# Kernel optimization log

Hardware: AMD Instinct MI355X
Metric: run time of the kernel (lower is better)

The kernel has to match this reference:

```python
import jax, jax.numpy as jnp
import numpy as np

B, N, CQ, H, CH = 1, 256, 128, 4, 32  # batch, n_res, c_q(=c_k=c_v), heads, per-head dim


def setup_inputs() -> dict:
    key = jax.random.key(0)
    ks = jax.random.split(key, 12)
    s = 0.02
    q_x = jax.random.normal(ks[0], (B, N, N, CQ), jnp.float32)
    kv_x = jax.random.normal(ks[1], (B, N, N, CQ), jnp.float32)
    # mask bias: 0 where kept, -1e9 where masked (additive mask)
    keep = jax.random.uniform(ks[2], (B, N, 1, 1, N)) < 0.9
    mask_bias = jnp.where(keep, 0.0, -1e9).astype(jnp.float32)
    triangle_bias = jax.random.normal(ks[3], (B, 1, H, N, N), jnp.float32)
    # projection weights, stored per-head as [H, CH, C_in]
    wq = jax.random.normal(ks[4], (H, CH, CQ), jnp.float32) * s
    wk = jax.random.normal(ks[5], (H, CH, CQ), jnp.float32) * s
    wv = jax.random.normal(ks[6], (H, CH, CQ), jnp.float32) * s
    wg = jax.random.normal(ks[7], (H, CH, CQ), jnp.float32) * s
    bg = jax.random.normal(ks[8], (H, CH), jnp.float32) * s + 1.0  # gating bias init 1
    wo = jax.random.normal(ks[9], (CQ, H * CH), jnp.float32) * s
    bo = jnp.zeros((CQ,), jnp.float32)
    return {"q_x": q_x, "kv_x": kv_x, "mask_bias": mask_bias,
            "triangle_bias": triangle_bias, "wq": wq, "wk": wk, "wv": wv,
            "wg": wg, "bg": bg, "wo": wo, "bo": bo}


def reference(q_x, kv_x, mask_bias, triangle_bias, wq, wk, wv, wg, bg, wo, bo):
    scale = 1.0 / np.sqrt(CH).astype(np.float32)
    # project + split heads: [B,N,Q,C] x [H,D,C] -> [B,N,H,Q,D]
    q = jnp.einsum('bnqc,hdc->bnhqd', q_x, wq) * scale
    k = jnp.einsum('bnkc,hdc->bnhkd', kv_x, wk)
    v = jnp.einsum('bnkc,hdc->bnhkd', kv_x, wv)
    # scores + additive biases (mask_bias broadcasts over h,q; triangle over n)
    a = jnp.einsum('bnhqd,bnhkd->bnhqk', q, k) + mask_bias + triangle_bias
    a = jax.nn.softmax(a, axis=-1)
    o = jnp.einsum('bnhqk,bnhkd->bnhqd', a, v)
    o = jnp.swapaxes(o, -2, -3)  # [B,N,Q,H,D]
    # gating
    g = jax.nn.sigmoid(jnp.einsum('bnqc,hdc->bnqhd', q_x, wg) + bg)
    o = o * g
    o = o.reshape(o.shape[:-2] + (H * CH,))  # [B,N,Q,H*D]
    return jnp.einsum('bnqe,ce->bnqc', o, wo) + bo
```

## Files before the change

### kernel.cpp

```cpp
#include <hip/hip_runtime.h>

#define NRES 256
#define CIN  128
#define NH   4
#define DH   32

typedef __attribute__((ext_vector_type(4))) float f32x4;
typedef __attribute__((ext_vector_type(8))) short bf16x8;

__device__ __forceinline__ short f2bf(float f) {
    unsigned u = __builtin_bit_cast(unsigned, f);
    u = (u + 0x7fffu + ((u >> 16) & 1u)) >> 16;
    return (short)u;
}

__device__ __forceinline__ bf16x8 ldcvt8(const float* __restrict__ p, float sc) {
    float4 a = *(const float4*)p;
    float4 b = *(const float4*)(p + 4);
    bf16x8 r;
    r[0] = f2bf(a.x * sc); r[1] = f2bf(a.y * sc); r[2] = f2bf(a.z * sc); r[3] = f2bf(a.w * sc);
    r[4] = f2bf(b.x * sc); r[5] = f2bf(b.y * sc); r[6] = f2bf(b.z * sc); r[7] = f2bf(b.w * sc);
    return r;
}

#define MFMA(a, b, c) __builtin_amdgcn_mfma_f32_16x16x32_bf16((a), (b), (c), 0, 0, 0)

__global__ __launch_bounds__(256, 2) void attn_mfma(
    const float* __restrict__ q_x, const float* __restrict__ kv_x,
    const float* __restrict__ mask_bias, const float* __restrict__ tri_bias,
    const float* __restrict__ wq, const float* __restrict__ wk,
    const float* __restrict__ wv, float* __restrict__ o_out)
{
    const int h = blockIdx.x, n = blockIdx.y;
    const int t = threadIdx.x;
    const int lane = t & 63, w = t >> 6;
    const int mrow = lane & 15;
    const int grp  = lane >> 4;
    const int koff = grp * 8;
    const int rbase = grp * 4;
    const int q0 = w * 64;

    __shared__ unsigned short Qs[NRES * DH];
    __shared__ unsigned short Ks[NRES * DH];
    __shared__ unsigned short Vt[DH * NRES];
    __shared__ unsigned short Pt[4 * 16 * 32];
    __shared__ float msk[NRES];

    if (t < 64) *(float4*)&msk[t * 4] = *(const float4*)(mask_bias + n * NRES + t * 4);

    const float* __restrict__ qxn  = q_x  + (size_t)n * NRES * CIN;
    const float* __restrict__ kxn  = kv_x + (size_t)n * NRES * CIN;
    const float* __restrict__ wqh  = wq + h * DH * CIN;
    const float* __restrict__ wkh  = wk + h * DH * CIN;
    const float* __restrict__ wvh  = wv + h * DH * CIN;
    const float* __restrict__ trih = tri_bias + (size_t)h * NRES * NRES;

    {
        const float qsc = 0.17677669529663687f;
        f32x4 aq_[4][2], ak_[4][2], av_[4][2];
        const f32x4 zf = {0.f, 0.f, 0.f, 0.f};
        #pragma unroll
        for (int qt = 0; qt < 4; ++qt)
            for (int dt = 0; dt < 2; ++dt) { aq_[qt][dt] = zf; ak_[qt][dt] = zf; av_[qt][dt] = zf; }

        #pragma unroll
        for (int ct = 0; ct < 4; ++ct) {
            const int c0 = ct * 32 + koff;
            bf16x8 bq0 = ldcvt8(wqh + mrow * CIN + c0, qsc);
            bf16x8 bq1 = ldcvt8(wqh + (16 + mrow) * CIN + c0, qsc);
            bf16x8 bk0 = ldcvt8(wkh + mrow * CIN + c0, 1.f);
            bf16x8 bk1 = ldcvt8(wkh + (16 + mrow) * CIN + c0, 1.f);
            bf16x8 bv0 = ldcvt8(wvh + mrow * CIN + c0, 1.f);
            bf16x8 bv1 = ldcvt8(wvh + (16 + mrow) * CIN + c0, 1.f);
            #pragma unroll
            for (int qt = 0; qt < 4; ++qt) {
                bf16x8 aX = ldcvt8(qxn + (q0 + qt * 16 + mrow) * CIN + c0, 1.f);
                aq_[qt][0] = MFMA(aX, bq0, aq_[qt][0]);
                aq_[qt][1] = MFMA(aX, bq1, aq_[qt][1]);
                bf16x8 aK = ldcvt8(kxn + (q0 + qt * 16 + mrow) * CIN + c0, 1.f);
                ak_[qt][0] = MFMA(aK, bk0, ak_[qt][0]);
                ak_[qt][1] = MFMA(aK, bk1, ak_[qt][1]);
                av_[qt][0] = MFMA(aK, bv0, av_[qt][0]);
                av_[qt][1] = MFMA(aK, bv1, av_[qt][1]);
            }
        }
        #pragma unroll
        for (int qt = 0; qt < 4; ++qt)
            #pragma unroll
            for (int dt = 0; dt < 2; ++dt)
                #pragma unroll
                for (int r = 0; r < 4; ++r) {
                    const int row = q0 + qt * 16 + rbase + r;
                    const int d = dt * 16 + mrow;
                    Qs[row * DH + d]   = (unsigned short)f2bf(aq_[qt][dt][r]);
                    Ks[row * DH + d]   = (unsigned short)f2bf(ak_[qt][dt][r]);
                    Vt[d * NRES + row] = (unsigned short)f2bf(av_[qt][dt][r]);
                }
    }
    __syncthreads();

    bf16x8 aq[4];
    #pragma unroll
    for (int qt = 0; qt < 4; ++qt)
        aq[qt] = *(const bf16x8*)&Qs[(q0 + qt * 16 + mrow) * DH + koff];

    f32x4 oa[4][2];
    f32x4 ls[4];
    const f32x4 zf = {0.f, 0.f, 0.f, 0.f};
    #pragma unroll
    for (int qt = 0; qt < 4; ++qt) { oa[qt][0] = zf; oa[qt][1] = zf; ls[qt] = zf; }

    unsigned short* __restrict__ pw = &Pt[w * 512];

    for (int kt = 0; kt < 8; ++kt) {
        const int kb = kt * 32;
        bf16x8 bk0 = *(const bf16x8*)&Ks[(kb + mrow) * DH + koff];
        bf16x8 bk1 = *(const bf16x8*)&Ks[(kb + 16 + mrow) * DH + koff];
        bf16x8 bv0 = *(const bf16x8*)&Vt[mrow * NRES + kb + koff];
        bf16x8 bv1 = *(const bf16x8*)&Vt[(16 + mrow) * NRES + kb + koff];
        const float mb0 = msk[kb + mrow];
        const float mb1 = msk[kb + 16 + mrow];

        #pragma unroll
        for (int qt = 0; qt < 4; ++qt) {
            f32x4 s0 = MFMA(aq[qt], bk0, zf);
            f32x4 s1 = MFMA(aq[qt], bk1, zf);
            const float* __restrict__ trow =
                trih + (q0 + qt * 16 + rbase) * NRES + kb + mrow;
            #pragma unroll
            for (int r = 0; r < 4; ++r) {
                s0[r] = __expf(s0[r] + mb0 + trow[r * NRES]      - 8.f);
                s1[r] = __expf(s1[r] + mb1 + trow[r * NRES + 16] - 8.f);
            }
            ls[qt] += s0 + s1;
            #pragma unroll
            for (int r = 0; r < 4; ++r) {
                pw[(rbase + r) * 32 + mrow]      = (unsigned short)f2bf(s0[r]);
                pw[(rbase + r) * 32 + 16 + mrow] = (unsigned short)f2bf(s1[r]);
            }
            asm volatile("s_waitcnt lgkmcnt(0)" ::: "memory");
            bf16x8 pa = *(const bf16x8*)&pw[mrow * 32 + koff];
            oa[qt][0] = MFMA(pa, bv0, oa[qt][0]);
            oa[qt][1] = MFMA(pa, bv1, oa[qt][1]);
        }
    }

    float* __restrict__ orow = o_out + (size_t)n * NRES * CIN + h * DH;
    #pragma unroll
    for (int qt = 0; qt < 4; ++qt) {
        f32x4 lv = ls[qt];
        #pragma unroll
        for (int xm = 1; xm < 16; xm <<= 1) {
            lv[0] += __shfl_xor(lv[0], xm, 64);
            lv[1] += __shfl_xor(lv[1], xm, 64);
            lv[2] += __shfl_xor(lv[2], xm, 64);
            lv[3] += __shfl_xor(lv[3], xm, 64);
        }
        #pragma unroll
        for (int r = 0; r < 4; ++r) {
            const float iv = 1.f / lv[r];
            const int q = q0 + qt * 16 + rbase + r;
            orow[q * CIN + mrow]      = oa[qt][0][r] * iv;
            orow[q * CIN + 16 + mrow] = oa[qt][1][r] * iv;
        }
    }
}

__global__ __launch_bounds__(256, 2) void gate_out(
    const float* __restrict__ q_x, const float* __restrict__ wg,
    const float* __restrict__ bg, const float* __restrict__ wo,
    const float* __restrict__ bo, float* __restrict__ io)
{
    const int t = threadIdx.x;
    const int tn = t & 31;
    const int tm = t >> 5;
    const int r0 = blockIdx.x * 64;

    __shared__ float As[64 * 128];
    __shared__ float Bs[16 * 128];

    {
        const int row = t >> 2, c0 = (t & 3) * 32;
        const float* __restrict__ src = q_x + (size_t)(r0 + row) * CIN + c0;
        #pragma unroll
        for (int p = 0; p < 8; ++p)
            *(float4*)&As[row * 128 + c0 + p * 4] = *(const float4*)(src + p * 4);
    }
    __syncthreads();

    float acc[8][4];
    #pragma unroll
    for (int i = 0; i < 8; ++i)
        #pragma unroll
        for (int j = 0; j < 4; ++j) acc[i][j] = 0.f;

    for (int kc = 0; kc < 8; ++kc) {
        {
            const int e = t >> 1, ch = (t & 1) * 8;
            const float* __restrict__ sw = wg + e * CIN + kc * 16 + ch;
            float4 v0 = *(const float4*)sw, v1 = *(const float4*)(sw + 4);
            Bs[(ch + 0) * 128 + e] = v0.x; Bs[(ch + 1) * 128 + e] = v0.y;
            Bs[(ch + 2) * 128 + e] = v0.z; Bs[(ch + 3) * 128 + e] = v0.w;
            Bs[(ch + 4) * 128 + e] = v1.x; Bs[(ch + 5) * 128 + e] = v1.y;
            Bs[(ch + 6) * 128 + e] = v1.z; Bs[(ch + 7) * 128 + e] = v1.w;
        }
        __syncthreads();
        #pragma unroll
        for (int kk = 0; kk < 16; ++kk) {
            float4 b4 = *(const float4*)&Bs[kk * 128 + tn * 4];
            #pragma unroll
            for (int i = 0; i < 8; ++i) {
                const float a = As[(tm * 8 + i) * 128 + kc * 16 + kk];
                acc[i][0] += a * b4.x; acc[i][1] += a * b4.y;
                acc[i][2] += a * b4.z; acc[i][3] += a * b4.w;
            }
        }
        __syncthreads();
    }

    float4 bg4 = *(const float4*)(bg + tn * 4);
    float gated[8][4];
    #pragma unroll
    for (int i = 0; i < 8; ++i) {
        float4 ov = *(const float4*)(io + (size_t)(r0 + tm * 8 + i) * CIN + tn * 4);
        const float o_[4] = {ov.x, ov.y, ov.z, ov.w};
        const float b_[4] = {bg4.x, bg4.y, bg4.z, bg4.w};
        #pragma unroll
        for (int j = 0; j < 4; ++j) {
            const float g = 1.f / (1.f + __expf(-(acc[i][j] + b_[j])));
            gated[i][j] = o_[j] * g;
        }
    }
    __syncthreads();
    #pragma unroll
    for (int i = 0; i < 8; ++i)
        *(float4*)&As[(tm * 8 + i) * 128 + tn * 4] =
            make_float4(gated[i][0], gated[i][1], gated[i][2], gated[i][3]);
    __syncthreads();

    float acc2[8][4];
    #pragma unroll
    for (int i = 0; i < 8; ++i)
        #pragma unroll
        for (int j = 0; j < 4; ++j) acc2[i][j] = 0.f;

    for (int kc = 0; kc < 8; ++kc) {
        {
            const int c = t >> 1, eh = (t & 1) * 8;
            const float* __restrict__ sw = wo + c * 128 + kc * 16 + eh;
            float4 v0 = *(const float4*)sw, v1 = *(const float4*)(sw + 4);
            Bs[(eh + 0) * 128 + c] = v0.x; Bs[(eh + 1) * 128 + c] = v0.y;
            Bs[(eh + 2) * 128 + c] = v0.z; Bs[(eh + 3) * 128 + c] = v0.w;
            Bs[(eh + 4) * 128 + c] = v1.x; Bs[(eh + 5) * 128 + c] = v1.y;
            Bs[(eh + 6) * 128 + c] = v1.z; Bs[(eh + 7) * 128 + c] = v1.w;
        }
        __syncthreads();
        #pragma unroll
        for (int kk = 0; kk < 16; ++kk) {
            float4 b4 = *(const float4*)&Bs[kk * 128 + tn * 4];
            #pragma unroll
            for (int i = 0; i < 8; ++i) {
                const float a = As[(tm * 8 + i) * 128 + kc * 16 + kk];
                acc2[i][0] += a * b4.x; acc2[i][1] += a * b4.y;
                acc2[i][2] += a * b4.z; acc2[i][3] += a * b4.w;
            }
        }
        __syncthreads();
    }

    float4 bo4 = *(const float4*)(bo + tn * 4);
    #pragma unroll
    for (int i = 0; i < 8; ++i) {
        float4 v = make_float4(acc2[i][0] + bo4.x, acc2[i][1] + bo4.y,
                               acc2[i][2] + bo4.z, acc2[i][3] + bo4.w);
        *(float4*)(io + (size_t)(r0 + tm * 8 + i) * CIN + tn * 4) = v;
    }
}

extern "C" void kernel_launch(void* const* d_in, const int* in_sizes, int n_in,
                              void* d_out, int out_size, void* d_ws, size_t ws_size,
                              hipStream_t stream) {
    const float* q_x  = (const float*)d_in[0];
    const float* kv_x = (const float*)d_in[1];
    const float* mask = (const float*)d_in[2];
    const float* tri  = (const float*)d_in[3];
    const float* wq   = (const float*)d_in[4];
    const float* wk   = (const float*)d_in[5];
    const float* wv   = (const float*)d_in[6];
    const float* wg   = (const float*)d_in[7];
    const float* bg   = (const float*)d_in[8];
    const float* wo   = (const float*)d_in[9];
    const float* bo   = (const float*)d_in[10];
    float* out = (float*)d_out;

    attn_mfma<<<dim3(NH, NRES), 256, 0, stream>>>(q_x, kv_x, mask, tri, wq, wk, wv, out);
    gate_out<<<(NRES * NRES) / 64, 256, 0, stream>>>(q_x, wg, bg, wo, bo, out);
}
```

Before: 263.0 us.

## Port gate/output projection to bf16 MFMA and restructure attention LDS usage

The gating and output projection kernel moves from a scalar fp32 shared-memory GEMM to bf16 MFMA, with gated activations staged per wave in padded LDS and launched with 128 rows per block. The attention kernel drops the shared Q buffer and passes Q through per-wave scratch instead. It also pads the V and P LDS strides, batches the triangle-bias loads ahead of the score MFMAs, packs bf16 conversions with perm, and raises the occupancy hint. The gate path gives up fp32 accuracy for bf16 matmuls, and the weights are reloaded from global memory for every tile.

```diff
diff --git a/kernel.cpp b/kernel.cpp
--- a/kernel.cpp
+++ b/kernel.cpp
@@ -5,27 +5,43 @@
 #define NH   4
 #define DH   32
 
+#define KST 32
+#define VST 264
+#define PST 40
+#define GST 136
+
 typedef __attribute__((ext_vector_type(4))) float f32x4;
 typedef __attribute__((ext_vector_type(8))) short bf16x8;
 
-__device__ __forceinline__ short f2bf(float f) {
+__device__ __forceinline__ unsigned pkbf(float a, float b) {
+    unsigned ua = __builtin_bit_cast(unsigned, a);
+    unsigned ub = __builtin_bit_cast(unsigned, b);
+    ua += 0x7fffu + ((ua >> 16) & 1u);
+    ub += 0x7fffu + ((ub >> 16) & 1u);
+    return __builtin_amdgcn_perm(ub, ua, 0x07060302);
+}
+__device__ __forceinline__ unsigned short f2bfu(float f) {
     unsigned u = __builtin_bit_cast(unsigned, f);
-    u = (u + 0x7fffu + ((u >> 16) & 1u)) >> 16;
-    return (short)u;
-}
-
-__device__ __forceinline__ bf16x8 ldcvt8(const float* __restrict__ p, float sc) {
-    float4 a = *(const float4*)p;
-    float4 b = *(const float4*)(p + 4);
-    bf16x8 r;
-    r[0] = f2bf(a.x * sc); r[1] = f2bf(a.y * sc); r[2] = f2bf(a.z * sc); r[3] = f2bf(a.w * sc);
-    r[4] = f2bf(b.x * sc); r[5] = f2bf(b.y * sc); r[6] = f2bf(b.z * sc); r[7] = f2bf(b.w * sc);
-    return r;
-}
-
+    return (unsigned short)((u + 0x7fffu + ((u >> 16) & 1u)) >> 16);
+}
+union bfr { unsigned u[4]; bf16x8 v; };
+__device__ __forceinline__ bf16x8 ldcvt8(const float* __restrict__ p) {
+    f32x4 a = *(const f32x4*)p; f32x4 b = *(const f32x4*)(p + 4);
+    bfr r;
+    r.u[0] = pkbf(a[0], a[1]); r.u[1] = pkbf(a[2], a[3]);
+    r.u[2] = pkbf(b[0], b[1]); r.u[3] = pkbf(b[2], b[3]);
+    return r.v;
+}
+__device__ __forceinline__ bf16x8 ldcvt8s(const float* __restrict__ p, float sc) {
+    f32x4 a = *(const f32x4*)p; f32x4 b = *(const f32x4*)(p + 4);
+    bfr r;
+    r.u[0] = pkbf(a[0] * sc, a[1] * sc); r.u[1] = pkbf(a[2] * sc, a[3] * sc);
+    r.u[2] = pkbf(b[0] * sc, b[1] * sc); r.u[3] = pkbf(b[2] * sc, b[3] * sc);
+    return r.v;
+}
 #define MFMA(a, b, c) __builtin_amdgcn_mfma_f32_16x16x32_bf16((a), (b), (c), 0, 0, 0)
 
-__global__ __launch_bounds__(256, 2) void attn_mfma(
+__global__ __launch_bounds__(256, 3) void attn_mfma(
     const float* __restrict__ q_x, const float* __restrict__ kv_x,
     const float* __restrict__ mask_bias, const float* __restrict__ tri_bias,
     const float* __restrict__ wq, const float* __restrict__ wk,
@@ -40,115 +56,143 @@
     const int rbase = grp * 4;
     const int q0 = w * 64;
 
-    __shared__ unsigned short Qs[NRES * DH];
-    __shared__ unsigned short Ks[NRES * DH];
-    __shared__ unsigned short Vt[DH * NRES];
-    __shared__ unsigned short Pt[4 * 16 * 32];
+    __shared__ unsigned short Ks[NRES * KST];
+    __shared__ unsigned short Vt[DH * VST];
+    __shared__ unsigned short Pt[4 * 32 * PST];
     __shared__ float msk[NRES];
 
     if (t < 64) *(float4*)&msk[t * 4] = *(const float4*)(mask_bias + n * NRES + t * 4);
 
-    const float* __restrict__ qxn  = q_x  + (size_t)n * NRES * CIN;
-    const float* __restrict__ kxn  = kv_x + (size_t)n * NRES * CIN;
-    const float* __restrict__ wqh  = wq + h * DH * CIN;
-    const float* __restrict__ wkh  = wk + h * DH * CIN;
-    const float* __restrict__ wvh  = wv + h * DH * CIN;
-    const float* __restrict__ trih = tri_bias + (size_t)h * NRES * NRES;
-
-    {
-        const float qsc = 0.17677669529663687f;
-        f32x4 aq_[4][2], ak_[4][2], av_[4][2];
-        const f32x4 zf = {0.f, 0.f, 0.f, 0.f};
-        #pragma unroll
-        for (int qt = 0; qt < 4; ++qt)
-            for (int dt = 0; dt < 2; ++dt) { aq_[qt][dt] = zf; ak_[qt][dt] = zf; av_[qt][dt] = zf; }
-
-        #pragma unroll
-        for (int ct = 0; ct < 4; ++ct) {
-            const int c0 = ct * 32 + koff;
-            bf16x8 bq0 = ldcvt8(wqh + mrow * CIN + c0, qsc);
-            bf16x8 bq1 = ldcvt8(wqh + (16 + mrow) * CIN + c0, qsc);
-            bf16x8 bk0 = ldcvt8(wkh + mrow * CIN + c0, 1.f);
-            bf16x8 bk1 = ldcvt8(wkh + (16 + mrow) * CIN + c0, 1.f);
-            bf16x8 bv0 = ldcvt8(wvh + mrow * CIN + c0, 1.f);
-            bf16x8 bv1 = ldcvt8(wvh + (16 + mrow) * CIN + c0, 1.f);
-            #pragma unroll
-            for (int qt = 0; qt < 4; ++qt) {
-                bf16x8 aX = ldcvt8(qxn + (q0 + qt * 16 + mrow) * CIN + c0, 1.f);
-                aq_[qt][0] = MFMA(aX, bq0, aq_[qt][0]);
-                aq_[qt][1] = MFMA(aX, bq1, aq_[qt][1]);
-                bf16x8 aK = ldcvt8(kxn + (q0 + qt * 16 + mrow) * CIN + c0, 1.f);
-                ak_[qt][0] = MFMA(aK, bk0, ak_[qt][0]);
-                ak_[qt][1] = MFMA(aK, bk1, ak_[qt][1]);
-                av_[qt][0] = MFMA(aK, bv0, av_[qt][0]);
-                av_[qt][1] = MFMA(aK, bv1, av_[qt][1]);
-            }
-        }
-        #pragma unroll
-        for (int qt = 0; qt < 4; ++qt)
+    const float* __restrict__ qxn = q_x  + (size_t)n * NRES * CIN;
+    const float* __restrict__ kxn = kv_x + (size_t)n * NRES * CIN;
+    const float* __restrict__ wqh = wq + h * DH * CIN;
+    const float* __restrict__ wkh = wk + h * DH * CIN;
+    const float* __restrict__ wvh = wv + h * DH * CIN;
+
+    f32x4 aq_[4][2], ak_[4][2], av_[4][2];
+    const f32x4 zf = {0.f, 0.f, 0.f, 0.f};
+    #pragma unroll
+    for (int qt = 0; qt < 4; ++qt)
+        #pragma unroll
+        for (int dt = 0; dt < 2; ++dt) { aq_[qt][dt] = zf; ak_[qt][dt] = zf; av_[qt][dt] = zf; }
+
+    const float qsc = 0.17677669529663687f;
+    #pragma unroll
+    for (int ct = 0; ct < 4; ++ct) {
+        const int c0 = ct * 32 + koff;
+        bf16x8 bq0 = ldcvt8s(wqh + mrow * CIN + c0, qsc);
+        bf16x8 bq1 = ldcvt8s(wqh + (16 + mrow) * CIN + c0, qsc);
+        bf16x8 bk0 = ldcvt8(wkh + mrow * CIN + c0);
+        bf16x8 bk1 = ldcvt8(wkh + (16 + mrow) * CIN + c0);
+        bf16x8 bv0 = ldcvt8(wvh + mrow * CIN + c0);
+        bf16x8 bv1 = ldcvt8(wvh + (16 + mrow) * CIN + c0);
+        #pragma unroll
+        for (int qt = 0; qt < 4; ++qt) {
+            bf16x8 aX = ldcvt8(qxn + (q0 + qt * 16 + mrow) * CIN + c0);
+            aq_[qt][0] = MFMA(aX, bq0, aq_[qt][0]);
+            aq_[qt][1] = MFMA(aX, bq1, aq_[qt][1]);
+            bf16x8 aK = ldcvt8(kxn + (q0 + qt * 16 + mrow) * CIN + c0);
+            ak_[qt][0] = MFMA(aK, bk0, ak_[qt][0]);
+            ak_[qt][1] = MFMA(aK, bk1, ak_[qt][1]);
+            av_[qt][0] = MFMA(aK, bv0, av_[qt][0]);
+            av_[qt][1] = MFMA(aK, bv1, av_[qt][1]);
+        }
+    }
+
+    #pragma unroll
+    for (int qt = 0; qt < 4; ++qt)
+        #pragma unroll
+        for (int dt = 0; dt < 2; ++dt)
+            #pragma unroll
+            for (int r = 0; r < 4; ++r) {
+                const int row = q0 + qt * 16 + rbase + r;
+                const int d = dt * 16 + mrow;
+                Ks[row * KST + d] = f2bfu(ak_[qt][dt][r]);
+                Vt[d * VST + row] = f2bfu(av_[qt][dt][r]);
+            }
+
+    unsigned short* __restrict__ pw = &Pt[w * 32 * PST];
+    bf16x8 aq[4];
+    #pragma unroll
+    for (int h2 = 0; h2 < 2; ++h2) {
+        #pragma unroll
+        for (int j = 0; j < 2; ++j) {
+            const int qt = h2 * 2 + j;
             #pragma unroll
             for (int dt = 0; dt < 2; ++dt)
                 #pragma unroll
-                for (int r = 0; r < 4; ++r) {
-                    const int row = q0 + qt * 16 + rbase + r;
-                    const int d = dt * 16 + mrow;
-                    Qs[row * DH + d]   = (unsigned short)f2bf(aq_[qt][dt][r]);
-                    Ks[row * DH + d]   = (unsigned short)f2bf(ak_[qt][dt][r]);
-                    Vt[d * NRES + row] = (unsigned short)f2bf(av_[qt][dt][r]);
-                }
+                for (int r = 0; r < 4; ++r)
+                    pw[(j * 16 + rbase + r) * PST + dt * 16 + mrow] = f2bfu(aq_[qt][dt][r]);
+        }
+        asm volatile("s_waitcnt lgkmcnt(0)" ::: "memory");
+        #pragma unroll
+        for (int j = 0; j < 2; ++j)
+            aq[h2 * 2 + j] = *(const bf16x8*)&pw[(j * 16 + mrow) * PST + koff];
+        asm volatile("s_waitcnt lgkmcnt(0)" ::: "memory");
     }
     __syncthreads();
 
-    bf16x8 aq[4];
-    #pragma unroll
-    for (int qt = 0; qt < 4; ++qt)
-        aq[qt] = *(const bf16x8*)&Qs[(q0 + qt * 16 + mrow) * DH + koff];
-
-    f32x4 oa[4][2];
-    f32x4 ls[4];
-    const f32x4 zf = {0.f, 0.f, 0.f, 0.f};
-    #pragma unroll
-    for (int qt = 0; qt < 4; ++qt) { oa[qt][0] = zf; oa[qt][1] = zf; ls[qt] = zf; }
-
-    unsigned short* __restrict__ pw = &Pt[w * 512];
+    f32x4 oa[4][2], ls4[4];
+    #pragma unroll
+    for (int qt = 0; qt < 4; ++qt) { oa[qt][0] = zf; oa[qt][1] = zf; ls4[qt] = zf; }
+
+    const float* __restrict__ trih = tri_bias + (size_t)h * NRES * NRES;
 
     for (int kt = 0; kt < 8; ++kt) {
         const int kb = kt * 32;
-        bf16x8 bk0 = *(const bf16x8*)&Ks[(kb + mrow) * DH + koff];
-        bf16x8 bk1 = *(const bf16x8*)&Ks[(kb + 16 + mrow) * DH + koff];
-        bf16x8 bv0 = *(const bf16x8*)&Vt[mrow * NRES + kb + koff];
-        bf16x8 bv1 = *(const bf16x8*)&Vt[(16 + mrow) * NRES + kb + koff];
-        const float mb0 = msk[kb + mrow];
-        const float mb1 = msk[kb + 16 + mrow];
-
-        #pragma unroll
-        for (int qt = 0; qt < 4; ++qt) {
-            f32x4 s0 = MFMA(aq[qt], bk0, zf);
-            f32x4 s1 = MFMA(aq[qt], bk1, zf);
-            const float* __restrict__ trow =
-                trih + (q0 + qt * 16 + rbase) * NRES + kb + mrow;
-            #pragma unroll
-            for (int r = 0; r < 4; ++r) {
-                s0[r] = __expf(s0[r] + mb0 + trow[r * NRES]      - 8.f);
-                s1[r] = __expf(s1[r] + mb1 + trow[r * NRES + 16] - 8.f);
-            }
-            ls[qt] += s0 + s1;
-            #pragma unroll
-            for (int r = 0; r < 4; ++r) {
-                pw[(rbase + r) * 32 + mrow]      = (unsigned short)f2bf(s0[r]);
-                pw[(rbase + r) * 32 + 16 + mrow] = (unsigned short)f2bf(s1[r]);
+        bf16x8 bk0 = *(const bf16x8*)&Ks[(kb + mrow) * KST + koff];
+        bf16x8 bk1 = *(const bf16x8*)&Ks[(kb + 16 + mrow) * KST + koff];
+        bf16x8 bv0 = *(const bf16x8*)&Vt[mrow * VST + kb + koff];
+        bf16x8 bv1 = *(const bf16x8*)&Vt[(16 + mrow) * VST + kb + koff];
+        const float mb0 = msk[kb + mrow] - 8.f;
+        const float mb1 = msk[kb + 16 + mrow] - 8.f;
+
+        #pragma unroll
+        for (int h2 = 0; h2 < 2; ++h2) {
+            float tr0[2][4], tr1[2][4];
+            #pragma unroll
+            for (int j = 0; j < 2; ++j) {
+                const int qt = h2 * 2 + j;
+                const float* __restrict__ trow =
+                    trih + (q0 + qt * 16 + rbase) * NRES + kb + mrow;
+                #pragma unroll
+                for (int r = 0; r < 4; ++r) {
+                    tr0[j][r] = trow[r * NRES];
+                    tr1[j][r] = trow[r * NRES + 16];
+                }
+            }
+            #pragma unroll
+            for (int j = 0; j < 2; ++j) {
+                const int qt = h2 * 2 + j;
+                f32x4 s0 = MFMA(aq[qt], bk0, zf);
+                f32x4 s1 = MFMA(aq[qt], bk1, zf);
+                #pragma unroll
+                for (int r = 0; r < 4; ++r) {
+                    s0[r] = __expf(s0[r] + tr0[j][r] + mb0);
+                    s1[r] = __expf(s1[r] + tr1[j][r] + mb1);
+                }
+                ls4[qt] += s0 + s1;
+                #pragma unroll
+                for (int r = 0; r < 4; ++r) {
+                    pw[(j * 16 + rbase + r) * PST + mrow]      = f2bfu(s0[r]);
+                    pw[(j * 16 + rbase + r) * PST + 16 + mrow] = f2bfu(s1[r]);
+                }
             }
             asm volatile("s_waitcnt lgkmcnt(0)" ::: "memory");
-            bf16x8 pa = *(const bf16x8*)&pw[mrow * 32 + koff];
-            oa[qt][0] = MFMA(pa, bv0, oa[qt][0]);
-            oa[qt][1] = MFMA(pa, bv1, oa[qt][1]);
+            #pragma unroll
+            for (int j = 0; j < 2; ++j) {
+                const int qt = h2 * 2 + j;
+                bf16x8 pa = *(const bf16x8*)&pw[(j * 16 + mrow) * PST + koff];
+                oa[qt][0] = MFMA(pa, bv0, oa[qt][0]);
+                oa[qt][1] = MFMA(pa, bv1, oa[qt][1]);
+            }
         }
     }
 
     float* __restrict__ orow = o_out + (size_t)n * NRES * CIN + h * DH;
     #pragma unroll
     for (int qt = 0; qt < 4; ++qt) {
-        f32x4 lv = ls[qt];
+        f32x4 lv = ls4[qt];
         #pragma unroll
         for (int xm = 1; xm < 16; xm <<= 1) {
             lv[0] += __shfl_xor(lv[0], xm, 64);
@@ -158,122 +202,91 @@
         }
         #pragma unroll
         for (int r = 0; r < 4; ++r) {
-            const float iv = 1.f / lv[r];
+            const float inv = 1.f / lv[r];
             const int q = q0 + qt * 16 + rbase + r;
-            orow[q * CIN + mrow]      = oa[qt][0][r] * iv;
-            orow[q * CIN + 16 + mrow] = oa[qt][1][r] * iv;
-        }
-    }
-}
-
-__global__ __launch_bounds__(256, 2) void gate_out(
+            orow[q * CIN + mrow]      = oa[qt][0][r] * inv;
+            orow[q * CIN + 16 + mrow] = oa[qt][1][r] * inv;
+        }
+    }
+}
+
+__global__ __launch_bounds__(256, 4) void gate_out(
     const float* __restrict__ q_x, const float* __restrict__ wg,
     const float* __restrict__ bg, const float* __restrict__ wo,
     const float* __restrict__ bo, float* __restrict__ io)
 {
     const int t = threadIdx.x;
-    const int tn = t & 31;
-    const int tm = t >> 5;
-    const int r0 = blockIdx.x * 64;
-
-    __shared__ float As[64 * 128];
-    __shared__ float Bs[16 * 128];
-
-    {
-        const int row = t >> 2, c0 = (t & 3) * 32;
-        const float* __restrict__ src = q_x + (size_t)(r0 + row) * CIN + c0;
-        #pragma unroll
-        for (int p = 0; p < 8; ++p)
-            *(float4*)&As[row * 128 + c0 + p * 4] = *(const float4*)(src + p * 4);
-    }
-    __syncthreads();
-
-    float acc[8][4];
-    #pragma unroll
-    for (int i = 0; i < 8; ++i)
-        #pragma unroll
-        for (int j = 0; j < 4; ++j) acc[i][j] = 0.f;
-
-    for (int kc = 0; kc < 8; ++kc) {
-        {
-            const int e = t >> 1, ch = (t & 1) * 8;
-            const float* __restrict__ sw = wg + e * CIN + kc * 16 + ch;
-            float4 v0 = *(const float4*)sw, v1 = *(const float4*)(sw + 4);
-            Bs[(ch + 0) * 128 + e] = v0.x; Bs[(ch + 1) * 128 + e] = v0.y;
-            Bs[(ch + 2) * 128 + e] = v0.z; Bs[(ch + 3) * 128 + e] = v0.w;
-            Bs[(ch + 4) * 128 + e] = v1.x; Bs[(ch + 5) * 128 + e] = v1.y;
-            Bs[(ch + 6) * 128 + e] = v1.z; Bs[(ch + 7) * 128 + e] = v1.w;
-        }
-        __syncthreads();
-        #pragma unroll
-        for (int kk = 0; kk < 16; ++kk) {
-            float4 b4 = *(const float4*)&Bs[kk * 128 + tn * 4];
-            #pragma unroll
-            for (int i = 0; i < 8; ++i) {
-                const float a = As[(tm * 8 + i) * 128 + kc * 16 + kk];
-                acc[i][0] += a * b4.x; acc[i][1] += a * b4.y;
-                acc[i][2] += a * b4.z; acc[i][3] += a * b4.w;
-            }
-        }
-        __syncthreads();
-    }
-
-    float4 bg4 = *(const float4*)(bg + tn * 4);
-    float gated[8][4];
-    #pragma unroll
-    for (int i = 0; i < 8; ++i) {
-        float4 ov = *(const float4*)(io + (size_t)(r0 + tm * 8 + i) * CIN + tn * 4);
-        const float o_[4] = {ov.x, ov.y, ov.z, ov.w};
-        const float b_[4] = {bg4.x, bg4.y, bg4.z, bg4.w};
-        #pragma unroll
-        for (int j = 0; j < 4; ++j) {
-            const float g = 1.f / (1.f + __expf(-(acc[i][j] + b_[j])));
-            gated[i][j] = o_[j] * g;
-        }
-    }
-    __syncthreads();
-    #pragma unroll
-    for (int i = 0; i < 8; ++i)
-        *(float4*)&As[(tm * 8 + i) * 128 + tn * 4] =
-            make_float4(gated[i][0], gated[i][1], gated[i][2], gated[i][3]);
-    __syncthreads();
-
-    float acc2[8][4];
-    #pragma unroll
-    for (int i = 0; i < 8; ++i)
-        #pragma unroll
-        for (int j = 0; j < 4; ++j) acc2[i][j] = 0.f;
-
-    for (int kc = 0; kc < 8; ++kc) {
-        {
-            const int c = t >> 1, eh = (t & 1) * 8;
-            const float* __restrict__ sw = wo + c * 128 + kc * 16 + eh;
-            float4 v0 = *(const float4*)sw, v1 = *(const float4*)(sw + 4);
-            Bs[(eh + 0) * 128 + c] = v0.x; Bs[(eh + 1) * 128 + c] = v0.y;
-            Bs[(eh + 2) * 128 + c] = v0.z; Bs[(eh + 3) * 128 + c] = v0.w;
-            Bs[(eh + 4) * 128 + c] = v1.x; Bs[(eh + 5) * 128 + c] = v1.y;
-            Bs[(eh + 6) * 128 + c] = v1.z; Bs[(eh + 7) * 128 + c] = v1.w;
-        }
-        __syncthreads();
-        #pragma unroll
-        for (int kk = 0; kk < 16; ++kk) {
-            float4 b4 = *(const float4*)&Bs[kk * 128 + tn * 4];
-            #pragma unroll
-            for (int i = 0; i < 8; ++i) {
-                const float a = As[(tm * 8 + i) * 128 + kc * 16 + kk];
-                acc2[i][0] += a * b4.x; acc2[i][1] += a * b4.y;
-                acc2[i][2] += a * b4.z; acc2[i][3] += a * b4.w;
-            }
-        }
-        __syncthreads();
-    }
-
-    float4 bo4 = *(const float4*)(bo + tn * 4);
-    #pragma unroll
-    for (int i = 0; i < 8; ++i) {
-        float4 v = make_float4(acc2[i][0] + bo4.x, acc2[i][1] + bo4.y,
-                               acc2[i][2] + bo4.z, acc2[i][3] + bo4.w);
-        *(float4*)(io + (size_t)(r0 + tm * 8 + i) * CIN + tn * 4) = v;
+    const int lane = t & 63, w = t >> 6;
+    const int mrow = lane & 15, grp = lane >> 4;
+    const int koff = grp * 8, rbase = grp * 4;
+    const int r0 = blockIdx.x * 128 + w * 32;
+
+    __shared__ unsigned short Gt[4 * 32 * GST];
+    unsigned short* __restrict__ gw = &Gt[w * 32 * GST];
+
+    const f32x4 zf = {0.f, 0.f, 0.f, 0.f};
+    f32x4 acc[2][8];
+    #pragma unroll
+    for (int at = 0; at < 2; ++at)
+        #pragma unroll
+        for (int nt = 0; nt < 8; ++nt) acc[at][nt] = zf;
+
+    #pragma unroll
+    for (int ks = 0; ks < 4; ++ks) {
+        const int c0 = ks * 32 + koff;
+        bf16x8 ax0 = ldcvt8(q_x + (size_t)(r0 + mrow) * CIN + c0);
+        bf16x8 ax1 = ldcvt8(q_x + (size_t)(r0 + 16 + mrow) * CIN + c0);
+        #pragma unroll
+        for (int nt = 0; nt < 8; ++nt) {
+            bf16x8 bw = ldcvt8(wg + (nt * 16 + mrow) * CIN + c0);
+            acc[0][nt] = MFMA(ax0, bw, acc[0][nt]);
+            acc[1][nt] = MFMA(ax1, bw, acc[1][nt]);
+        }
+    }
+
+    #pragma unroll
+    for (int nt = 0; nt < 8; ++nt) {
+        const float bge = bg[nt * 16 + mrow];
+        #pragma unroll
+        for (int at = 0; at < 2; ++at)
+            #pragma unroll
+            for (int r = 0; r < 4; ++r) {
+                const int qg = r0 + at * 16 + rbase + r;
+                const float ov = io[(size_t)qg * CIN + nt * 16 + mrow];
+                const float g = 1.f / (1.f + __expf(-(acc[at][nt][r] + bge)));
+                gw[(at * 16 + rbase + r) * GST + nt * 16 + mrow] = f2bfu(ov * g);
+            }
+    }
+    asm volatile("s_waitcnt lgkmcnt(0)" ::: "memory");
+
+    f32x4 acc2[2][8];
+    #pragma unroll
+    for (int at = 0; at < 2; ++at)
+        #pragma unroll
+        for (int nt = 0; nt < 8; ++nt) acc2[at][nt] = zf;
+
+    #pragma unroll
+    for (int ks = 0; ks < 4; ++ks) {
+        const int e0 = ks * 32 + koff;
+        bf16x8 ag0 = *(const bf16x8*)&gw[mrow * GST + e0];
+        bf16x8 ag1 = *(const bf16x8*)&gw[(16 + mrow) * GST + e0];
+        #pragma unroll
+        for (int nt = 0; nt < 8; ++nt) {
+            bf16x8 bw = ldcvt8(wo + (nt * 16 + mrow) * CIN + e0);
+            acc2[0][nt] = MFMA(ag0, bw, acc2[0][nt]);
+            acc2[1][nt] = MFMA(ag1, bw, acc2[1][nt]);
+        }
+    }
+
+    #pragma unroll
+    for (int nt = 0; nt < 8; ++nt) {
+        const float boc = bo[nt * 16 + mrow];
+        #pragma unroll
+        for (int at = 0; at < 2; ++at)
+            #pragma unroll
+            for (int r = 0; r < 4; ++r)
+                io[(size_t)(r0 + at * 16 + rbase + r) * CIN + nt * 16 + mrow] =
+                    acc2[at][nt][r] + boc;
     }
 }
 
@@ -294,5 +307,5 @@
     float* out = (float*)d_out;
 
     attn_mfma<<<dim3(NH, NRES), 256, 0, stream>>>(q_x, kv_x, mask, tri, wq, wk, wv, out);
-    gate_out<<<(NRES * NRES) / 64, 256, 0, stream>>>(q_x, wg, bg, wo, bo, out);
-}
+    gate_out<<<(NRES * NRES) / 128, 256, 0, stream>>>(q_x, wg, bg, wo, bo, out);
+}
```

Measured after the change: 270.6 us. 2.9% more time.
